# Optimization experiments

Measured on AMD Instinct MI355X. Metric: run time of the kernel, lower is better.

The kernel has to match this reference:

```python
import jax, jax.numpy as jnp
import numpy as np

WINDOW_SIZES = (4, 8, 16)
STRIDE_FACTOR = 0.5
EPS = 1e-6


def _pool_scale(x, mask_f, w, stride):
    # x: [B,T,D], mask_f: [B,T] float. Overlapping masked mean via prefix sums.
    B, T, D = x.shape
    xm = x * mask_f[:, :, None]
    cx = jnp.concatenate([jnp.zeros((B, 1, D), x.dtype), jnp.cumsum(xm, axis=1)], axis=1)  # [B,T+1,D]
    cm = jnp.concatenate([jnp.zeros((B, 1), x.dtype), jnp.cumsum(mask_f, axis=1)], axis=1)  # [B,T+1]
    starts = jnp.arange(0, T - w + 1, stride)  # [S]
    num = cx[:, starts + w, :] - cx[:, starts, :]          # [B,S,D] masked window sums
    valid = cm[:, starts + w] - cm[:, starts]              # [B,S] valid counts
    avg = num / jnp.clip(valid, EPS)[:, :, None]
    return avg, valid > 0


def setup_inputs() -> dict:
    key = jax.random.key(0)
    k1, k2 = jax.random.split(key)
    B, T, D = 8, 4096, 512
    x = jax.random.normal(k1, (B, T, D), dtype=jnp.float32)
    mask = jax.random.bernoulli(k2, 0.9, (B, T))  # bool, True=valid
    return {"x": x, "mask": mask}


def reference(x, mask):
    mask_f = mask.astype(x.dtype)
    vis_list, msk_list = [], []
    for w in WINDOW_SIZES:
        stride = max(1, int(w * STRIDE_FACTOR))
        avg, m = _pool_scale(x, mask_f, w, stride)
        vis_list.append(avg)
        msk_list.append(m)
    return (*vis_list, *msk_list)
```

## Files before the change

kernel.cpp:

```cpp
#include <hip/hip_runtime.h>


#define EPS 1e-6f

typedef float f4 __attribute__((ext_vector_type(4)));

constexpr int B = 8, T = 4096, D = 512, D4 = D / 4;
constexpr int TILE = 32;
constexpr int HALO = 8;
constexpr int NT = TILE + HALO;
constexpr int NP = NT / 2;
constexpr int NTILES = T / TILE;
constexpr int S4 = 2047, S8 = 1023, S16 = 511;

constexpr size_t OFF0 = 0;
constexpr size_t OFF1 = (size_t)B * S4 * D;
constexpr size_t OFF2 = OFF1 + (size_t)B * S8 * D;
constexpr size_t OFF3 = OFF2 + (size_t)B * S16 * D;
constexpr size_t OFF4 = OFF3 + (size_t)B * S4;
constexpr size_t OFF5 = OFF4 + (size_t)B * S8;

template <bool GUARD>
__device__ __forceinline__ void tile_body(const f4* __restrict__ x4,
                                          const int* __restrict__ mask,
                                          float* __restrict__ out, int b,
                                          int tile, int d4, int lane,
                                          bool write_masks) {
  const int t0 = tile * TILE;

  const int* mp = mask + (size_t)b * T + t0;
  float mf[NT];
#pragma unroll
  for (int i = 0; i < NT; ++i) {
    int m = (!GUARD || (t0 + i) < T) ? mp[i] : 0;
    mf[i] = (m != 0) ? 1.0f : 0.0f;
  }

  float c2[NP];
#pragma unroll
  for (int i = 0; i < NP; ++i) c2[i] = mf[2 * i] + mf[2 * i + 1];
  float c4[19];
#pragma unroll
  for (int j = 0; j < 19; ++j) c4[j] = c2[j] + c2[j + 1];
  float c8[9];
#pragma unroll
  for (int k = 0; k < 9; ++k) c8[k] = c4[2 * k] + c4[2 * k + 2];
  float c16[4];
#pragma unroll
  for (int l = 0; l < 4; ++l) c16[l] = c8[2 * l] + c8[2 * l + 2];

  float i4[16], i8[8], i16[4];
#pragma unroll
  for (int j = 0; j < 16; ++j) i4[j] = 1.0f / fmaxf(c4[j], EPS);
#pragma unroll
  for (int k = 0; k < 8; ++k) i8[k] = 1.0f / fmaxf(c8[k], EPS);
#pragma unroll
  for (int l = 0; l < 4; ++l) i16[l] = 1.0f / fmaxf(c16[l], EPS);

  if (write_masks) {
    if (lane < 16) {
      int s = tile * 16 + lane;
      if (!GUARD || s < S4) {
        float c = 0.f;
#pragma unroll
        for (int j = 0; j < 16; ++j) c = (lane == j) ? c4[j] : c;
        out[OFF3 + (size_t)b * S4 + s] = (c > 0.f) ? 1.f : 0.f;
      }
    } else if (lane < 24) {
      int k = lane - 16, s = tile * 8 + k;
      if (!GUARD || s < S8) {
        float c = 0.f;
#pragma unroll
        for (int j = 0; j < 8; ++j) c = (k == j) ? c8[j] : c;
        out[OFF4 + (size_t)b * S8 + s] = (c > 0.f) ? 1.f : 0.f;
      }
    } else if (lane < 28) {
      int l = lane - 24, s = tile * 4 + l;
      if (!GUARD || s < S16) {
        float c = 0.f;
#pragma unroll
        for (int j = 0; j < 4; ++j) c = (l == j) ? c16[j] : c;
        out[OFF5 + (size_t)b * S16 + s] = (c > 0.f) ? 1.f : 0.f;
      }
    }
  }

  const f4* xb = x4 + (size_t)b * T * D4 + d4;
  f4 p[NP];
#pragma unroll
  for (int i = 0; i < NP; ++i) {
    int t = t0 + 2 * i;
    f4 a0 = {0.f, 0.f, 0.f, 0.f}, a1 = {0.f, 0.f, 0.f, 0.f};
    if (!GUARD || t < T) {
      a0 = xb[(size_t)t * D4];
      a1 = xb[(size_t)(t + 1) * D4];
    }
    p[i] = a0 * mf[2 * i] + a1 * mf[2 * i + 1];
  }

  f4 q4[19];
#pragma unroll
  for (int j = 0; j < 19; ++j) q4[j] = p[j] + p[j + 1];
  f4 q8[9];
#pragma unroll
  for (int k = 0; k < 9; ++k) q8[k] = q4[2 * k] + q4[2 * k + 2];

  f4* o4 = (f4*)(out + OFF0) + ((size_t)b * S4 + (size_t)tile * 16) * D4 + d4;
#pragma unroll
  for (int j = 0; j < 16; ++j) {
    if (!GUARD || (tile * 16 + j) < S4) {
      f4 v = q4[j] * i4[j];
      __builtin_nontemporal_store(v, o4 + (size_t)j * D4);
    }
  }

  f4* o8 = (f4*)(out + OFF1) + ((size_t)b * S8 + (size_t)tile * 8) * D4 + d4;
#pragma unroll
  for (int k = 0; k < 8; ++k) {
    if (!GUARD || (tile * 8 + k) < S8) {
      f4 v = q8[k] * i8[k];
      __builtin_nontemporal_store(v, o8 + (size_t)k * D4);
    }
  }

  f4* o16 = (f4*)(out + OFF2) + ((size_t)b * S16 + (size_t)tile * 4) * D4 + d4;
#pragma unroll
  for (int l = 0; l < 4; ++l) {
    if (!GUARD || (tile * 4 + l) < S16) {
      f4 v = (q8[2 * l] + q8[2 * l + 2]) * i16[l];
      __builtin_nontemporal_store(v, o16 + (size_t)l * D4);
    }
  }
}

__global__ __launch_bounds__(64)
void tpp_kernel(const f4* __restrict__ x4, const int* __restrict__ mask,
                float* __restrict__ out) {
  const int lane = threadIdx.x;
  const int d4 = blockIdx.x * 64 + lane;
  const int b = blockIdx.z;
  const int tile = blockIdx.y;
  const bool write_masks = (blockIdx.x == 0);

  if (tile < NTILES - 1)
    tile_body<false>(x4, mask, out, b, tile, d4, lane, write_masks);
  else
    tile_body<true>(x4, mask, out, b, tile, d4, lane, write_masks);
}

extern "C" void kernel_launch(void* const* d_in, const int* in_sizes, int n_in,
                              void* d_out, int out_size, void* d_ws,
                              size_t ws_size, hipStream_t stream) {
  const f4* x4 = (const f4*)d_in[0];
  const int* mask = (const int*)d_in[1];
  float* out = (float*)d_out;
  dim3 grid(D4 / 64, NTILES, B);
  tpp_kernel<<<grid, 64, 0, stream>>>(x4, mask, out);
}
```

Measured before the change: 109.4 us.

## Split window scales across warps in 256-thread blocks with fast reciprocal

Reorganizes the kernel so each 256-thread block covers the full D range of a tile. Two waves compute the window-4 outputs and two waves compute the window-8/16 outputs, each half of D. The goal is to shorten each wave's register-heavy dependency chain and raise occupancy. It also replaces IEEE division with the hardware approximate reciprocal. The cost is that x is now read twice per tile, once by the w4 waves and once by the w8/16 waves, and the approximate reciprocal may slightly change numerics.

```diff
diff --git a/kernel.cpp b/kernel.cpp
--- a/kernel.cpp
+++ b/kernel.cpp
@@ -7,9 +7,6 @@
 
 constexpr int B = 8, T = 4096, D = 512, D4 = D / 4;
 constexpr int TILE = 32;
-constexpr int HALO = 8;
-constexpr int NT = TILE + HALO;
-constexpr int NP = NT / 2;
 constexpr int NTILES = T / TILE;
 constexpr int S4 = 2047, S8 = 1023, S16 = 511;
 
@@ -20,62 +17,96 @@
 constexpr size_t OFF4 = OFF3 + (size_t)B * S4;
 constexpr size_t OFF5 = OFF4 + (size_t)B * S8;
 
+__device__ __forceinline__ float rcp_clip(float c) {
+  return __builtin_amdgcn_rcpf(fmaxf(c, EPS));
+}
+
 template <bool GUARD>
-__device__ __forceinline__ void tile_body(const f4* __restrict__ x4,
-                                          const int* __restrict__ mask,
-                                          float* __restrict__ out, int b,
-                                          int tile, int d4, int lane,
-                                          bool write_masks) {
+__device__ __forceinline__ void w4_body(const f4* __restrict__ xb,
+                                        const int* __restrict__ mp,
+                                        float* __restrict__ out, int b,
+                                        int tile, int d4, int lane,
+                                        bool wmask) {
   const int t0 = tile * TILE;
-
-  const int* mp = mask + (size_t)b * T + t0;
-  float mf[NT];
+  float mf[34];
 #pragma unroll
-  for (int i = 0; i < NT; ++i) {
+  for (int i = 0; i < 34; ++i) {
     int m = (!GUARD || (t0 + i) < T) ? mp[i] : 0;
     mf[i] = (m != 0) ? 1.0f : 0.0f;
   }
+  float c4[16];
+#pragma unroll
+  for (int j = 0; j < 16; ++j)
+    c4[j] = (mf[2 * j] + mf[2 * j + 1]) + (mf[2 * j + 2] + mf[2 * j + 3]);
 
-  float c2[NP];
+  if (wmask && lane < 16) {
+    int s = tile * 16 + lane;
+    if (!GUARD || s < S4) {
+      float c = 0.f;
 #pragma unroll
-  for (int i = 0; i < NP; ++i) c2[i] = mf[2 * i] + mf[2 * i + 1];
-  float c4[19];
+      for (int j = 0; j < 16; ++j) c = (lane == j) ? c4[j] : c;
+      out[OFF3 + (size_t)b * S4 + s] = (c > 0.f) ? 1.f : 0.f;
+    }
+  }
+
+  f4 p[17];
 #pragma unroll
-  for (int j = 0; j < 19; ++j) c4[j] = c2[j] + c2[j + 1];
+  for (int i = 0; i < 17; ++i) {
+    int t = t0 + 2 * i;
+    f4 a0 = {0.f, 0.f, 0.f, 0.f}, a1 = {0.f, 0.f, 0.f, 0.f};
+    if (!GUARD || t < T) {
+      a0 = xb[(size_t)t * D4];
+      a1 = xb[(size_t)(t + 1) * D4];
+    }
+    p[i] = a0 * mf[2 * i] + a1 * mf[2 * i + 1];
+  }
+
+  f4* o4 = (f4*)(out + OFF0) + ((size_t)b * S4 + (size_t)tile * 16) * D4 + d4;
+#pragma unroll
+  for (int j = 0; j < 16; ++j) {
+    if (!GUARD || (tile * 16 + j) < S4) {
+      f4 v = (p[j] + p[j + 1]) * rcp_clip(c4[j]);
+      __builtin_nontemporal_store(v, o4 + (size_t)j * D4);
+    }
+  }
+}
+
+template <bool GUARD>
+__device__ __forceinline__ void w816_body(const f4* __restrict__ xb,
+                                          const int* __restrict__ mp,
+                                          float* __restrict__ out, int b,
+                                          int tile, int d4, int lane,
+                                          bool wmask) {
+  const int t0 = tile * TILE;
+  float mf[40];
+#pragma unroll
+  for (int i = 0; i < 40; ++i) {
+    int m = (!GUARD || (t0 + i) < T) ? mp[i] : 0;
+    mf[i] = (m != 0) ? 1.0f : 0.0f;
+  }
   float c8[9];
 #pragma unroll
-  for (int k = 0; k < 9; ++k) c8[k] = c4[2 * k] + c4[2 * k + 2];
+  for (int k = 0; k < 9; ++k) {
+    float c = 0.f;
+#pragma unroll
+    for (int i = 0; i < 8; ++i) c += mf[4 * k + i];
+    c8[k] = c;
+  }
   float c16[4];
 #pragma unroll
   for (int l = 0; l < 4; ++l) c16[l] = c8[2 * l] + c8[2 * l + 2];
 
-  float i4[16], i8[8], i16[4];
-#pragma unroll
-  for (int j = 0; j < 16; ++j) i4[j] = 1.0f / fmaxf(c4[j], EPS);
-#pragma unroll
-  for (int k = 0; k < 8; ++k) i8[k] = 1.0f / fmaxf(c8[k], EPS);
-#pragma unroll
-  for (int l = 0; l < 4; ++l) i16[l] = 1.0f / fmaxf(c16[l], EPS);
-
-  if (write_masks) {
-    if (lane < 16) {
-      int s = tile * 16 + lane;
-      if (!GUARD || s < S4) {
-        float c = 0.f;
-#pragma unroll
-        for (int j = 0; j < 16; ++j) c = (lane == j) ? c4[j] : c;
-        out[OFF3 + (size_t)b * S4 + s] = (c > 0.f) ? 1.f : 0.f;
-      }
-    } else if (lane < 24) {
-      int k = lane - 16, s = tile * 8 + k;
+  if (wmask) {
+    if (lane < 8) {
+      int s = tile * 8 + lane;
       if (!GUARD || s < S8) {
         float c = 0.f;
 #pragma unroll
-        for (int j = 0; j < 8; ++j) c = (k == j) ? c8[j] : c;
+        for (int j = 0; j < 8; ++j) c = (lane == j) ? c8[j] : c;
         out[OFF4 + (size_t)b * S8 + s] = (c > 0.f) ? 1.f : 0.f;
       }
-    } else if (lane < 28) {
-      int l = lane - 24, s = tile * 4 + l;
+    } else if (lane < 12) {
+      int l = lane - 8, s = tile * 4 + l;
       if (!GUARD || s < S16) {
         float c = 0.f;
 #pragma unroll
@@ -85,10 +116,9 @@
     }
   }
 
-  const f4* xb = x4 + (size_t)b * T * D4 + d4;
-  f4 p[NP];
+  f4 p[20];
 #pragma unroll
-  for (int i = 0; i < NP; ++i) {
+  for (int i = 0; i < 20; ++i) {
     int t = t0 + 2 * i;
     f4 a0 = {0.f, 0.f, 0.f, 0.f}, a1 = {0.f, 0.f, 0.f, 0.f};
     if (!GUARD || t < T) {
@@ -98,27 +128,16 @@
     p[i] = a0 * mf[2 * i] + a1 * mf[2 * i + 1];
   }
 
-  f4 q4[19];
-#pragma unroll
-  for (int j = 0; j < 19; ++j) q4[j] = p[j] + p[j + 1];
   f4 q8[9];
 #pragma unroll
-  for (int k = 0; k < 9; ++k) q8[k] = q4[2 * k] + q4[2 * k + 2];
-
-  f4* o4 = (f4*)(out + OFF0) + ((size_t)b * S4 + (size_t)tile * 16) * D4 + d4;
-#pragma unroll
-  for (int j = 0; j < 16; ++j) {
-    if (!GUARD || (tile * 16 + j) < S4) {
-      f4 v = q4[j] * i4[j];
-      __builtin_nontemporal_store(v, o4 + (size_t)j * D4);
-    }
-  }
+  for (int k = 0; k < 9; ++k)
+    q8[k] = (p[2 * k] + p[2 * k + 1]) + (p[2 * k + 2] + p[2 * k + 3]);
 
   f4* o8 = (f4*)(out + OFF1) + ((size_t)b * S8 + (size_t)tile * 8) * D4 + d4;
 #pragma unroll
   for (int k = 0; k < 8; ++k) {
     if (!GUARD || (tile * 8 + k) < S8) {
-      f4 v = q8[k] * i8[k];
+      f4 v = q8[k] * rcp_clip(c8[k]);
       __builtin_nontemporal_store(v, o8 + (size_t)k * D4);
     }
   }
@@ -127,25 +146,38 @@
 #pragma unroll
   for (int l = 0; l < 4; ++l) {
     if (!GUARD || (tile * 4 + l) < S16) {
-      f4 v = (q8[2 * l] + q8[2 * l + 2]) * i16[l];
+      f4 v = (q8[2 * l] + q8[2 * l + 2]) * rcp_clip(c16[l]);
       __builtin_nontemporal_store(v, o16 + (size_t)l * D4);
     }
   }
 }
 
-__global__ __launch_bounds__(64)
+__global__ __launch_bounds__(256, 4)
 void tpp_kernel(const f4* __restrict__ x4, const int* __restrict__ mask,
                 float* __restrict__ out) {
-  const int lane = threadIdx.x;
-  const int d4 = blockIdx.x * 64 + lane;
+  const int tid = threadIdx.x;
+  const int wid = tid >> 6;
+  const int lane = tid & 63;
+  const int dhalf = wid & 1;
+  const int d4 = dhalf * 64 + lane;
   const int b = blockIdx.z;
   const int tile = blockIdx.y;
-  const bool write_masks = (blockIdx.x == 0);
 
-  if (tile < NTILES - 1)
-    tile_body<false>(x4, mask, out, b, tile, d4, lane, write_masks);
-  else
-    tile_body<true>(x4, mask, out, b, tile, d4, lane, write_masks);
+  const f4* xb = x4 + (size_t)b * T * D4 + d4;
+  const int* mp = mask + (size_t)b * T + tile * TILE;
+  const bool last = (tile == NTILES - 1);
+
+  if (wid < 2) {
+    if (!last)
+      w4_body<false>(xb, mp, out, b, tile, d4, lane, wid == 0);
+    else
+      w4_body<true>(xb, mp, out, b, tile, d4, lane, wid == 0);
+  } else {
+    if (!last)
+      w816_body<false>(xb, mp, out, b, tile, d4, lane, wid == 2);
+    else
+      w816_body<true>(xb, mp, out, b, tile, d4, lane, wid == 2);
+  }
 }
 
 extern "C" void kernel_launch(void* const* d_in, const int* in_sizes, int n_in,
@@ -154,6 +186,6 @@
   const f4* x4 = (const f4*)d_in[0];
   const int* mask = (const int*)d_in[1];
   float* out = (float*)d_out;
-  dim3 grid(D4 / 64, NTILES, B);
-  tpp_kernel<<<grid, 64, 0, stream>>>(x4, mask, out);
+  dim3 grid(1, NTILES, B);
+  tpp_kernel<<<grid, 256, 0, stream>>>(x4, mask, out);
 }
```

Result: slower. 114.9 us (+5.0%).
